# Kernel tuning notes

Measured on AMD Instinct MI355X. Metric: run time of the kernel, lower is better.

## Reference

```python
import jax, jax.numpy as jnp
import numpy as np

H = 1024          # hidden_size (hardcoded in module)
NB = 32           # nbones
D = 3 * NB        # 96 pose features
T_IN = 49         # input_window_size - 1 encoder steps
T_OUT = 25        # output_window_size
B = 512


def setup_inputs() -> dict:
    key = jax.random.key(0)
    ks = jax.random.split(key, 12)
    s = 1.0 / np.sqrt(H)  # PyTorch GRUCell default init scale
    u = lambda k, shape, sc: jax.random.uniform(k, shape, jnp.float32, -sc, sc)
    return {
        "encoder_inputs": jax.random.normal(ks[0], (B, T_IN, D), jnp.float32),
        "decoder_inputs": jax.random.normal(ks[1], (B, 1, D), jnp.float32),
        "enc_Wih": u(ks[2], (3 * H, D), s),
        "enc_Whh": u(ks[3], (3 * H, H), s),
        "enc_bih": u(ks[4], (3 * H,), s),
        "enc_bhh": u(ks[5], (3 * H,), s),
        "dec_Wih": u(ks[6], (3 * H, D), s),
        "dec_Whh": u(ks[7], (3 * H, H), s),
        "dec_bih": u(ks[8], (3 * H,), s),
        "dec_bhh": u(ks[9], (3 * H,), s),
        "W_out": u(ks[10], (H, D), 0.04),   # module inits uniform(-0.04, 0.04)
        "b_out": u(ks[11], (D,), 0.04),
    }


def gru_cell(x, h, Wih, Whh, bih, bhh):
    # PyTorch nn.GRUCell: gates ordered (r, z, n)
    gi = x @ Wih.T + bih          # [B, 3H]
    gh = h @ Whh.T + bhh          # [B, 3H]
    gir, giz, gin = jnp.split(gi, 3, axis=-1)
    ghr, ghz, ghn = jnp.split(gh, 3, axis=-1)
    r = jax.nn.sigmoid(gir + ghr)
    z = jax.nn.sigmoid(giz + ghz)
    n = jnp.tanh(gin + r * ghn)
    return (1.0 - z) * n + z * h


def reference(encoder_inputs, decoder_inputs,
              enc_Wih, enc_Whh, enc_bih, enc_bhh,
              dec_Wih, dec_Whh, dec_bih, dec_bhh,
              W_out, b_out):
    b = encoder_inputs.shape[0]
    dt = encoder_inputs.dtype

    # --- encoder: sequential GRU over T_IN frames (result unused by decoder,
    # faithfully matching the original module, which never consumes enc_state) ---
    def enc_step(h, x):
        return gru_cell(x, h, enc_Wih, enc_Whh, enc_bih, enc_bhh), None

    enc_state, _ = jax.lax.scan(enc_step, jnp.zeros((b, H), dt),
                                jnp.swapaxes(encoder_inputs, 0, 1))

    # first hidden is zeros (PyTorch GRUCell default when h not given) ---
    p = decoder_inputs[:, 0, :]

    def dec_step(carry, _):
        h, x = carry
        hn = gru_cell(x, h, dec_Wih, dec_Whh, dec_bih, dec_bhh)
        out = hn @ W_out + b_out
        return (hn, out), out

    _, outs = jax.lax.scan(dec_step, (jnp.zeros((b, H), dt), p),
                           None, length=T_OUT)
    prediction = jnp.swapaxes(outs, 0, 1)  # [B, T_OUT, D]
    return prediction
```

## Files before the change

### kernel.cpp

```cpp
#include <hip/hip_runtime.h>
#include <hip/hip_bf16.h>

typedef __attribute__((ext_vector_type(8))) short short8;
typedef __attribute__((ext_vector_type(4))) float f32x4;
typedef __attribute__((ext_vector_type(4))) unsigned u32x4;
typedef unsigned short u16;

#define BB 512
#define HH 1024
#define TT 25
#define CTB 128
#define HSZ (BB*HH)


__device__ __forceinline__ float sigm(float x){ return 1.f/(1.f+__expf(-x)); }
__device__ __forceinline__ float tanh_(float x){
  float e = __expf(-2.f*fabsf(x));
  float t = (1.f-e)/(1.f+e);
  return copysignf(t, x);
}
__device__ __forceinline__ u16 f2bf(float x){
  union { float f; unsigned u; } v; v.f = x;
  unsigned r = v.u + 0x7FFFu + ((v.u>>16)&1u);
  return (u16)(r>>16);
}
__device__ __forceinline__ void store16_wt(void* p, u32x4 v){
  asm volatile("global_store_dwordx4 %0, %1, off sc0 sc1" :: "v"(p), "v"(v) : "memory");
}
__device__ __forceinline__ void aload(short8 &d, const short8* p){
  asm volatile("global_load_dwordx4 %0, %1, off" : "=v"(d) : "v"(p));
}

#if __has_builtin(__builtin_amdgcn_global_load_lds)
#define GLOAD_LDS16(g, l) __builtin_amdgcn_global_load_lds( \
    (const __attribute__((address_space(1))) void*)(g), \
    (__attribute__((address_space(3))) void*)(l), 16, 0, 0)
#define HAVE_GLL 1
#else
#define HAVE_GLL 0
#endif

__device__ __forceinline__ size_t wc_idx(int ct, int r, int k){
  int nf = r>>4, rl = r&15, kit = k>>5, k31 = k&31;
  int lane = rl | (((k31>>3)&3)<<4);
  return (size_t)ct*49152 + ((size_t)(kit*3+nf)*64 + (size_t)lane)*8 + (k31&7);
}


__device__ void prep_wx_body(int bid, float* smem,
                             const float* __restrict__ Wih,
                             const float* __restrict__ Wout,
                             u16* __restrict__ Wcp){
  float (*sWih)[97] = (float(*)[97])smem;
  float (*sWo)[97]  = (float(*)[97])(smem + 32*97);
  int tid = threadIdx.x;
  int nt = bid % 96, kt = bid / 96;
  for (int i = tid; i < 32*96; i += 256){ int r2=i/96, d=i%96; sWih[r2][d] = Wih[(size_t)(nt*32+r2)*96 + d]; }
  for (int i = tid; i < 64*96; i += 256){ int r2=i/96, d=i%96; sWo[r2][d]  = Wout[(size_t)(kt*64+r2)*96 + d]; }
  __syncthreads();
  int ni = tid & 31, kb = tid >> 5;
  float acc[8];
  #pragma unroll
  for (int i=0;i<8;i++) acc[i]=0.f;
  for (int d = 0; d < 96; d++){
    float a = sWih[ni][d];
    #pragma unroll
    for (int i=0;i<8;i++) acc[i] += a * sWo[kb*8 + i][d];
  }
  int n = nt*32 + ni;
  int g = n >> 10, j = n & 1023;
  int ct = j >> 3, u = j & 7, r = g*8 + u;
  size_t base = wc_idx(ct, r, kt*64 + kb*8);
  #pragma unroll
  for (int i=0;i<8;i++) Wcp[base+i] = f2bf(acc[i]);
}

__device__ void prep_cast_body(int bid,
                               const float* __restrict__ Whh, const float* __restrict__ bhh,
                               const float* __restrict__ Wout,
                               u16* __restrict__ Wcp, float* __restrict__ cbias,
                               u16* __restrict__ WoT){
  int tid = threadIdx.x;
  if (bid < 3072){
    int g1 = bid >> 10, j = bid & 1023;
    int ct = j >> 3, u = j & 7, r = (3+g1)*8 + u;
    const float* src = Whh + (size_t)bid*1024;
    if (tid < 128){
      int k0 = tid*8;
      size_t base = wc_idx(ct, r, k0);
      #pragma unroll
      for (int i=0;i<8;i++) Wcp[base+i] = f2bf(src[k0+i]);
    }
    if (!tid) cbias[ct*48 + r] = bhh[bid];
  } else {
    int d = bid - 3072;
    for (int k = tid; k < 1024; k += 256)
      WoT[(size_t)d*1024 + k] = f2bf(Wout[(size_t)k*96 + d]);
  }
}

__device__ void prep_cx_body(int bid,
                             const float* __restrict__ Wih, const float* __restrict__ bih,
                             const float* __restrict__ bout, float* __restrict__ cbias){
  int n = bid*256 + threadIdx.x;
  if (n >= 3072) return;
  float acc = bih[n];
  const float* wrow = Wih + (size_t)n*96;
  for (int d = 0; d < 96; d++) acc += bout[d]*wrow[d];
  int g = n >> 10, j = n & 1023;
  cbias[(j>>3)*48 + g*8 + (j&7)] = acc;
}

__device__ void step0_body(int bid, float* smem,
                           const float* __restrict__ dec_in, const float* __restrict__ Wih,
                           const float* __restrict__ bih, const float* __restrict__ bhh,
                           float* __restrict__ h_f32, u16* __restrict__ h_bf,
                           unsigned* __restrict__ flags){
  if (bid == 0 && threadIdx.x < 256) flags[threadIdx.x] = 0u;
  float (*sP)[97] = (float(*)[97])smem;
  float (*sW)[97] = (float(*)[97])(smem + 64*97);
  int tid = threadIdx.x;
  int bt = bid & 7;
  int jt = bid >> 3;
  for (int i = tid; i < 64*96; i += 256){ int r=i/96, d=i%96; sP[r][d] = dec_in[(size_t)(bt*64+r)*96 + d]; }
  int tb = tid >> 4, tj = tid & 15;
  float gg[3][4][4];
  for (int g = 0; g < 3; g++){
    __syncthreads();
    for (int i = tid; i < 64*96; i += 256){ int r=i/96, d=i%96; sW[r][d] = Wih[((size_t)g*1024 + jt*64 + r)*96 + d]; }
    __syncthreads();
    float acc[4][4];
    #pragma unroll
    for (int x=0;x<4;x++)
      #pragma unroll
      for (int y=0;y<4;y++) acc[x][y]=0.f;
    for (int d = 0; d < 96; d++){
      float a[4], wv[4];
      #pragma unroll
      for (int x=0;x<4;x++) a[x]  = sP[tb + x*16][d];
      #pragma unroll
      for (int y=0;y<4;y++) wv[y] = sW[tj + y*16][d];
      #pragma unroll
      for (int x=0;x<4;x++)
        #pragma unroll
        for (int y=0;y<4;y++) acc[x][y] += a[x]*wv[y];
    }
    #pragma unroll
    for (int x=0;x<4;x++)
      #pragma unroll
      for (int y=0;y<4;y++) gg[g][x][y] = acc[x][y];
  }
  #pragma unroll
  for (int x=0;x<4;x++)
    #pragma unroll
    for (int y=0;y<4;y++){
      int b = bt*64 + tb + x*16;
      int j = jt*64 + tj + y*16;
      float gir = gg[0][x][y] + bih[j];
      float giz = gg[1][x][y] + bih[1024+j];
      float gin = gg[2][x][y] + bih[2048+j];
      float r = sigm(gir + bhh[j]);
      float z = sigm(giz + bhh[1024+j]);
      float nn = tanh_(gin + r*bhh[2048+j]);
      float h = (1.f - z)*nn;
      h_f32[(size_t)j*512 + b] = h;
      h_bf[(size_t)(((b>>4)*32 + (j>>5))*512 + (b&15)*32 + (j&31))] = f2bf(h);
    }
}

__global__ __launch_bounds__(256)
void k_prep_all(const float* __restrict__ dec_in,
                const float* __restrict__ Wih, const float* __restrict__ Whh,
                const float* __restrict__ bih, const float* __restrict__ bhh,
                const float* __restrict__ Wout, const float* __restrict__ bout,
                u16* __restrict__ Wcp, float* __restrict__ cbias,
                u16* __restrict__ WoT,
                float* __restrict__ hf0, u16* __restrict__ hb0,
                unsigned* __restrict__ flags){
  __shared__ float smem[2*64*97];
  int bid = blockIdx.x;
  if (bid < 1536)            prep_wx_body(bid, smem, Wih, Wout, Wcp);
  else if (bid < 4704)       prep_cast_body(bid-1536, Whh, bhh, Wout, Wcp, cbias, WoT);
  else if (bid < 4716)       prep_cx_body(bid-4704, Wih, bih, bout, cbias);
  else                       step0_body(bid-4716, smem, dec_in, Wih, bih, bhh, hf0, hb0, flags);
}

__global__ __launch_bounds__(256, 1)
void k_persist7(const float* __restrict__ hf0, u16* __restrict__ hbase,
                const u16* __restrict__ Wcp, const float* __restrict__ cbias,
                unsigned* __restrict__ flags){
  __shared__ short8 sB[6144];
  int b = blockIdx.x, tid = threadIdx.x;
  int lane = tid & 63, w = tid >> 6;
  int l16 = lane & 15, lk = lane >> 4;
  int r8 = b & 7;
  int bt = r8 >> 2;
  int ct = (b >> 3)*4 + (r8 & 3);

  const short8* Wblk = (const short8*)Wcp + (size_t)ct*6144;
#if HAVE_GLL
  #pragma unroll
  for (int it = 0; it < 24; it++){
    int i = it*256 + tid;
    GLOAD_LDS16(Wblk + i, &sB[i]);
  }
#else
  for (int i = tid; i < 6144; i += 256) sB[i] = Wblk[i];
#endif

  float c0 = cbias[ct*48 +  0 + l16];
  float c1 = cbias[ct*48 + 16 + l16];
  float c2 = cbias[ct*48 + 32 + l16];
  bool hiB = (l16 & 8) != 0;
  int rowA = bt*256 + w*64;
  int rb0 = rowA >> 4;
  int myFlag = bt*128 + ct;

  float hold[4][4];
  if (!hiB){
    int colg = ct*8 + l16;
    #pragma unroll
    for (int mf = 0; mf < 4; mf++){
      f32x4 h4 = *(const f32x4*)(hf0 + (size_t)colg*512 + rowA + mf*16 + lk*4);
      hold[mf][0]=h4[0]; hold[mf][1]=h4[1]; hold[mf][2]=h4[2]; hold[mf][3]=h4[3];
    }
  }
  __syncthreads();

  for (int t = 1; t <= 24; ++t){
    const short8* pin8 = (const short8*)(hbase + (size_t)(t-1)*HSZ);
    u16* pout = hbase + (size_t)t*HSZ;
    const short8* Ap = pin8 + (size_t)rb0*2048 + l16*4 + lk;

    short8 ar[4][4];
    #define AISSUE(k, s) { \
      aload(ar[s][0], Ap + 0*2048 + (k)*64); \
      aload(ar[s][1], Ap + 1*2048 + (k)*64); \
      aload(ar[s][2], Ap + 2*2048 + (k)*64); \
      aload(ar[s][3], Ap + 3*2048 + (k)*64); }

    AISSUE(0,0); AISSUE(1,1); AISSUE(2,2); AISSUE(3,3);

    short8 brw[2][3];
    #pragma unroll
    for (int nf = 0; nf < 3; nf++) brw[0][nf] = sB[nf*64 + lane];

    f32x4 acc[4][3];
    #pragma unroll
    for (int m=0;m<4;m++)
      #pragma unroll
      for (int nf=0;nf<3;nf++) acc[m][nf] = f32x4{0.f,0.f,0.f,0.f};

    #pragma unroll
    for (int kit = 0; kit < 32; kit++){
      const int cur = kit & 1, nxt = cur ^ 1, sa = kit & 3;
      if (kit <= 28)      asm volatile("s_waitcnt vmcnt(12)" ::: "memory");
      else if (kit == 29) asm volatile("s_waitcnt vmcnt(8)"  ::: "memory");
      else if (kit == 30) asm volatile("s_waitcnt vmcnt(4)"  ::: "memory");
      else                asm volatile("s_waitcnt vmcnt(0)"  ::: "memory");
      __builtin_amdgcn_sched_barrier(0);
      if (kit < 31){
        #pragma unroll
        for (int nf = 0; nf < 3; nf++) brw[nxt][nf] = sB[(kit+1)*192 + nf*64 + lane];
      }
      acc[0][0] = __builtin_amdgcn_mfma_f32_16x16x32_bf16(ar[sa][0], brw[cur][0], acc[0][0], 0,0,0);
      acc[1][0] = __builtin_amdgcn_mfma_f32_16x16x32_bf16(ar[sa][1], brw[cur][0], acc[1][0], 0,0,0);
      acc[2][0] = __builtin_amdgcn_mfma_f32_16x16x32_bf16(ar[sa][2], brw[cur][0], acc[2][0], 0,0,0);
      acc[3][0] = __builtin_amdgcn_mfma_f32_16x16x32_bf16(ar[sa][3], brw[cur][0], acc[3][0], 0,0,0);
      acc[0][1] = __builtin_amdgcn_mfma_f32_16x16x32_bf16(ar[sa][0], brw[cur][1], acc[0][1], 0,0,0);
      acc[1][1] = __builtin_amdgcn_mfma_f32_16x16x32_bf16(ar[sa][1], brw[cur][1], acc[1][1], 0,0,0);
      acc[2][1] = __builtin_amdgcn_mfma_f32_16x16x32_bf16(ar[sa][2], brw[cur][1], acc[2][1], 0,0,0);
      acc[3][1] = __builtin_amdgcn_mfma_f32_16x16x32_bf16(ar[sa][3], brw[cur][1], acc[3][1], 0,0,0);
      acc[0][2] = __builtin_amdgcn_mfma_f32_16x16x32_bf16(ar[sa][0], brw[cur][2], acc[0][2], 0,0,0);
      acc[1][2] = __builtin_amdgcn_mfma_f32_16x16x32_bf16(ar[sa][1], brw[cur][2], acc[1][2], 0,0,0);
      acc[2][2] = __builtin_amdgcn_mfma_f32_16x16x32_bf16(ar[sa][2], brw[cur][2], acc[2][2], 0,0,0);
      acc[3][2] = __builtin_amdgcn_mfma_f32_16x16x32_bf16(ar[sa][3], brw[cur][2], acc[3][2], 0,0,0);
      if (kit < 28) AISSUE(kit+4, sa);
    }
    #undef AISSUE

    #pragma unroll
    for (int mf=0; mf<4; mf++){
      #pragma unroll
      for (int j=0;j<4;j++){
        float g0 = acc[mf][0][j] + c0;
        float g1 = acc[mf][1][j] + c1;
        float g2 = acc[mf][2][j] + c2;
        float v1 = hiB ? g1 : g2;
        float w1 = __shfl_xor(v1, 8, 64);
        float rz = sigm(g0 + w1);
        float w2 = __shfl_xor(rz, 8, 64);
        float v3 = hiB ? (w2 * g2) : 0.f;
        float w3 = __shfl_xor(v3, 8, 64);
        float hnew = 0.f;
        if (!hiB){
          float nn = tanh_(g1 + w3);
          hnew = (1.f - w2)*nn + w2*hold[mf][j];
          hold[mf][j] = hnew;
        }
        float o1 = __shfl_xor(hnew, 1, 64);
        unsigned pk = ((unsigned)f2bf(o1) << 16) | (unsigned)f2bf(hnew);
        unsigned pk2 = __shfl_xor(pk, 2, 64);
        unsigned q2 = __shfl_xor(pk, 4, 64);
        unsigned q3 = __shfl_xor(pk2, 4, 64);
        if (l16 == 0){
          u32x4 vv = {pk, pk2, q2, q3};
          store16_wt((char*)pout + (size_t)(rb0+mf)*32768 + (size_t)(ct>>2)*1024
                                 + (size_t)(lk*4+j)*64 + (size_t)(ct&3)*16, vv);
        }
      }
    }

    __syncthreads();
    if (tid == 0)
      __hip_atomic_store(&flags[myFlag], (unsigned)t,
                         __ATOMIC_RELAXED, __HIP_MEMORY_SCOPE_AGENT);
    if (tid < 128){
      unsigned tgt = (unsigned)t;
      while (__hip_atomic_load(&flags[bt*128 + tid], __ATOMIC_RELAXED,
                               __HIP_MEMORY_SCOPE_AGENT) < tgt)
        __builtin_amdgcn_s_sleep(2);
    }
    __syncthreads();
  }
}

__global__ __launch_bounds__(384)
void k_pred(const u16* __restrict__ hbase, const u16* __restrict__ WoT,
            const float* __restrict__ bout, float* __restrict__ pred){
  int blk = blockIdx.x;
  int i = blk >> 5, rbt = blk & 31;
  int tid = threadIdx.x;
  int lane = tid & 63, bn = tid >> 6;
  int l16 = lane & 15, lk = lane >> 4;
  const short8* Aq = (const short8*)(hbase + (size_t)i*HSZ)
                     + (size_t)rbt*2048 + l16*4 + lk;
  const short8* Bq = (const short8*)WoT + (size_t)(bn*16 + l16)*128 + lk;
  f32x4 acc = {0.f,0.f,0.f,0.f};
  #pragma unroll 8
  for (int kit = 0; kit < 32; kit++)
    acc = __builtin_amdgcn_mfma_f32_16x16x32_bf16(Aq[kit*64], Bq[kit*4], acc, 0,0,0);
  int c = bn*16 + l16;
  float bb = bout[c];
  #pragma unroll
  for (int j=0;j<4;j++){
    int row = rbt*16 + lk*4 + j;
    pred[(size_t)row*2400 + (size_t)i*96 + c] = acc[j] + bb;
  }
}

extern "C" void kernel_launch(void* const* d_in, const int* in_sizes, int n_in,
                              void* d_out, int out_size, void* d_ws, size_t ws_size,
                              hipStream_t stream){
  const float* dec_in = (const float*)d_in[1];
  const float* Wih  = (const float*)d_in[6];
  const float* Whh  = (const float*)d_in[7];
  const float* bih  = (const float*)d_in[8];
  const float* bhh  = (const float*)d_in[9];
  const float* Wout = (const float*)d_in[10];
  const float* bout = (const float*)d_in[11];
  float* pred = (float*)d_out;

  char* ws = (char*)d_ws;
  size_t off = 0;
  u16* Wcp = (u16*)(ws + off);   off += (size_t)CTB*48*1024*2;
  u16* WoT = (u16*)(ws + off);   off += (size_t)96*1024*2;
  float* cbias = (float*)(ws + off); off += (size_t)6144*4;
  off = (off + 255) & ~(size_t)255;
  float* hf0 = (float*)(ws + off); off += (size_t)BB*HH*4;
  u16* hbase = (u16*)(ws + off);   off += (size_t)TT*HSZ*2;
  off = (off + 255) & ~(size_t)255;
  unsigned* flags = (unsigned*)(ws + off); off += 1024;

  k_prep_all<<<4844, 256, 0, stream>>>(dec_in, Wih, Whh, bih, bhh, Wout, bout,
                                       Wcp, cbias, WoT, hf0, hbase, flags);

  const float* hf0_c = hf0;
  void* kargs[] = {(void*)&hf0_c, (void*)&hbase, (void*)&Wcp, (void*)&cbias,
                   (void*)&flags};
  hipLaunchCooperativeKernel((const void*)k_persist7, dim3(256), dim3(256),
                             kargs, 0, stream);

  k_pred<<<800, 384, 0, stream>>>(hbase, WoT, bout, pred);
}
```

Before: 526.4 us.

## Split K across wave pairs in persistent GRU kernel with LDS reduction

Doubles the persistent kernel's block to 512 threads and splits each step's K=1024 reduction between two waves, each handling half of the K iterations. The partial accumulators are exchanged through a new shared-memory buffer, and each wave then runs the gate epilogue for half of the row fragments. This is meant to halve the serial MFMA chain per wave and add latency hiding on the critical recurrent path. The cost is an extra block barrier, added LDS traffic and more LDS use per step.

Measured after the change: 675.7 us. 28.4% more time.

```diff
diff --git a/kernel.cpp b/kernel.cpp
--- a/kernel.cpp
+++ b/kernel.cpp
@@ -185,14 +185,16 @@
   else                       step0_body(bid-4716, smem, dec_in, Wih, bih, bhh, hf0, hb0, flags);
 }
 
-__global__ __launch_bounds__(256, 1)
-void k_persist7(const float* __restrict__ hf0, u16* __restrict__ hbase,
+__global__ __launch_bounds__(512, 1)
+void k_persist8(const float* __restrict__ hf0, u16* __restrict__ hbase,
                 const u16* __restrict__ Wcp, const float* __restrict__ cbias,
                 unsigned* __restrict__ flags){
   __shared__ short8 sB[6144];
+  __shared__ f32x4 sRed[4][2][6][64];
   int b = blockIdx.x, tid = threadIdx.x;
   int lane = tid & 63, w = tid >> 6;
   int l16 = lane & 15, lk = lane >> 4;
+  int kh = w & 1, wr = w >> 1;
   int r8 = b & 7;
   int bt = r8 >> 2;
   int ct = (b >> 3)*4 + (r8 & 3);
@@ -200,29 +202,32 @@
   const short8* Wblk = (const short8*)Wcp + (size_t)ct*6144;
 #if HAVE_GLL
   #pragma unroll
-  for (int it = 0; it < 24; it++){
-    int i = it*256 + tid;
+  for (int it = 0; it < 12; it++){
+    int i = it*512 + tid;
     GLOAD_LDS16(Wblk + i, &sB[i]);
   }
 #else
-  for (int i = tid; i < 6144; i += 256) sB[i] = Wblk[i];
+  for (int i = tid; i < 6144; i += 512) sB[i] = Wblk[i];
 #endif
 
   float c0 = cbias[ct*48 +  0 + l16];
   float c1 = cbias[ct*48 + 16 + l16];
   float c2 = cbias[ct*48 + 32 + l16];
   bool hiB = (l16 & 8) != 0;
-  int rowA = bt*256 + w*64;
+  int rowA = bt*256 + wr*64;
   int rb0 = rowA >> 4;
   int myFlag = bt*128 + ct;
-
-  float hold[4][4];
+  const int gk0 = kh*16;
+  const int other = kh ^ 1;
+
+  float hold[2][4];
   if (!hiB){
     int colg = ct*8 + l16;
     #pragma unroll
-    for (int mf = 0; mf < 4; mf++){
+    for (int mo = 0; mo < 2; mo++){
+      int mf = kh*2 + mo;
       f32x4 h4 = *(const f32x4*)(hf0 + (size_t)colg*512 + rowA + mf*16 + lk*4);
-      hold[mf][0]=h4[0]; hold[mf][1]=h4[1]; hold[mf][2]=h4[2]; hold[mf][3]=h4[3];
+      hold[mo][0]=h4[0]; hold[mo][1]=h4[1]; hold[mo][2]=h4[2]; hold[mo][3]=h4[3];
     }
   }
   __syncthreads();
@@ -234,16 +239,16 @@
 
     short8 ar[4][4];
     #define AISSUE(k, s) { \
-      aload(ar[s][0], Ap + 0*2048 + (k)*64); \
-      aload(ar[s][1], Ap + 1*2048 + (k)*64); \
-      aload(ar[s][2], Ap + 2*2048 + (k)*64); \
-      aload(ar[s][3], Ap + 3*2048 + (k)*64); }
-
-    AISSUE(0,0); AISSUE(1,1); AISSUE(2,2); AISSUE(3,3);
+      aload(ar[s][0], Ap + 0*2048 + (size_t)(k)*64); \
+      aload(ar[s][1], Ap + 1*2048 + (size_t)(k)*64); \
+      aload(ar[s][2], Ap + 2*2048 + (size_t)(k)*64); \
+      aload(ar[s][3], Ap + 3*2048 + (size_t)(k)*64); }
+
+    AISSUE(gk0+0,0); AISSUE(gk0+1,1); AISSUE(gk0+2,2); AISSUE(gk0+3,3);
 
     short8 brw[2][3];
     #pragma unroll
-    for (int nf = 0; nf < 3; nf++) brw[0][nf] = sB[nf*64 + lane];
+    for (int nf = 0; nf < 3; nf++) brw[0][nf] = sB[gk0*192 + nf*64 + lane];
 
     f32x4 acc[4][3];
     #pragma unroll
@@ -252,16 +257,16 @@
       for (int nf=0;nf<3;nf++) acc[m][nf] = f32x4{0.f,0.f,0.f,0.f};
 
     #pragma unroll
-    for (int kit = 0; kit < 32; kit++){
-      const int cur = kit & 1, nxt = cur ^ 1, sa = kit & 3;
-      if (kit <= 28)      asm volatile("s_waitcnt vmcnt(12)" ::: "memory");
-      else if (kit == 29) asm volatile("s_waitcnt vmcnt(8)"  ::: "memory");
-      else if (kit == 30) asm volatile("s_waitcnt vmcnt(4)"  ::: "memory");
-      else                asm volatile("s_waitcnt vmcnt(0)"  ::: "memory");
+    for (int q = 0; q < 16; q++){
+      const int cur = q & 1, nxt = cur ^ 1, sa = q & 3;
+      if (q <= 12)      asm volatile("s_waitcnt vmcnt(12)" ::: "memory");
+      else if (q == 13) asm volatile("s_waitcnt vmcnt(8)"  ::: "memory");
+      else if (q == 14) asm volatile("s_waitcnt vmcnt(4)"  ::: "memory");
+      else              asm volatile("s_waitcnt vmcnt(0)"  ::: "memory");
       __builtin_amdgcn_sched_barrier(0);
-      if (kit < 31){
+      if (q < 15){
         #pragma unroll
-        for (int nf = 0; nf < 3; nf++) brw[nxt][nf] = sB[(kit+1)*192 + nf*64 + lane];
+        for (int nf = 0; nf < 3; nf++) brw[nxt][nf] = sB[(gk0+q+1)*192 + nf*64 + lane];
       }
       acc[0][0] = __builtin_amdgcn_mfma_f32_16x16x32_bf16(ar[sa][0], brw[cur][0], acc[0][0], 0,0,0);
       acc[1][0] = __builtin_amdgcn_mfma_f32_16x16x32_bf16(ar[sa][1], brw[cur][0], acc[1][0], 0,0,0);
@@ -275,12 +280,25 @@
       acc[1][2] = __builtin_amdgcn_mfma_f32_16x16x32_bf16(ar[sa][1], brw[cur][2], acc[1][2], 0,0,0);
       acc[2][2] = __builtin_amdgcn_mfma_f32_16x16x32_bf16(ar[sa][2], brw[cur][2], acc[2][2], 0,0,0);
       acc[3][2] = __builtin_amdgcn_mfma_f32_16x16x32_bf16(ar[sa][3], brw[cur][2], acc[3][2], 0,0,0);
-      if (kit < 28) AISSUE(kit+4, sa);
+      if (q < 12) AISSUE(gk0+q+4, sa);
     }
     #undef AISSUE
 
     #pragma unroll
-    for (int mf=0; mf<4; mf++){
+    for (int mo = 0; mo < 2; mo++)
+      #pragma unroll
+      for (int nf = 0; nf < 3; nf++)
+        sRed[wr][kh][mo*3+nf][lane] = acc[other*2+mo][nf];
+    __syncthreads();
+    #pragma unroll
+    for (int mo = 0; mo < 2; mo++)
+      #pragma unroll
+      for (int nf = 0; nf < 3; nf++)
+        acc[kh*2+mo][nf] += sRed[wr][other][mo*3+nf][lane];
+
+    #pragma unroll
+    for (int mo=0; mo<2; mo++){
+      int mf = kh*2 + mo;
       #pragma unroll
       for (int j=0;j<4;j++){
         float g0 = acc[mf][0][j] + c0;
@@ -295,8 +313,8 @@
         float hnew = 0.f;
         if (!hiB){
           float nn = tanh_(g1 + w3);
-          hnew = (1.f - w2)*nn + w2*hold[mf][j];
-          hold[mf][j] = hnew;
+          hnew = (1.f - w2)*nn + w2*hold[mo][j];
+          hold[mo][j] = hnew;
         }
         float o1 = __shfl_xor(hnew, 1, 64);
         unsigned pk = ((unsigned)f2bf(o1) << 16) | (unsigned)f2bf(hnew);
@@ -378,7 +396,7 @@
   const float* hf0_c = hf0;
   void* kargs[] = {(void*)&hf0_c, (void*)&hbase, (void*)&Wcp, (void*)&cbias,
                    (void*)&flags};
-  hipLaunchCooperativeKernel((const void*)k_persist7, dim3(256), dim3(256),
+  hipLaunchCooperativeKernel((const void*)k_persist8, dim3(256), dim3(512),
                              kargs, 0, stream);
 
   k_pred<<<800, 384, 0, stream>>>(hbase, WoT, bout, pred);
```
